# Kernel optimization log

Measured on AMD Instinct MI355X. Metric: run time of the kernel, lower is better.

## Reference

```python
import jax, jax.numpy as jnp
import numpy as np

TEMPERATURE = 0.2
EPS = 1e-8
N, D = 8192, 256
EDGE_PROB = 0.002  # ~16 neighbors per node


def setup_inputs() -> dict:
    key = jax.random.key(0)
    k1, k2, k3 = jax.random.split(key, 3)
    z_view = jax.random.normal(k1, (N, D), dtype=jnp.float32)
    z_fused = jax.random.normal(k2, (N, D), dtype=jnp.float32)
    # sparse binary fused-graph adjacency, densified (matches Gf_sparse.to_dense())
    Gf_dense = (jax.random.uniform(k3, (N, N)) < EDGE_PROB).astype(jnp.float32)
    return {"z_view": z_view, "z_fused": z_fused, "Gf_dense": Gf_dense}


def _l2_normalize(x, eps=1e-12):
    # matches F.normalize(p=2, dim=1): x / max(||x||, eps)
    norm = jnp.sqrt(jnp.sum(x * x, axis=1, keepdims=True))
    return x / jnp.maximum(norm, eps)


def reference(z_view, z_fused, Gf_dense):
    n = z_view.shape[0]
    zv = _l2_normalize(z_view)
    zf = _l2_normalize(z_fused)
    sim = jnp.matmul(zv, zf.T) / TEMPERATURE  # [N, N]
    eye = jnp.eye(n, dtype=sim.dtype)
    pos_mask = ((eye + Gf_dense) > 0).astype(sim.dtype)  # diag always 1
    neg_mask = 1.0 - pos_mask
    pos_scores = jnp.sum(sim * pos_mask, axis=1, keepdims=True) / (
        jnp.sum(pos_mask, axis=1, keepdims=True) + EPS
    )  # [N, 1]
    neg_scores = sim * neg_mask  # [N, N] (positive slots zeroed, kept as logits)
    logits = jnp.concatenate([pos_scores, neg_scores], axis=1)  # [N, N+1]
    # CrossEntropyLoss(reduction='sum') with labels == 0, then / N
    lse = jax.nn.logsumexp(logits, axis=1)
    loss = jnp.sum(lse - logits[:, 0]) / n
    return loss
```

## Files before the change

### kernel.cpp

```cpp
#include <hip/hip_runtime.h>

#define NROW 8192
#define DIM  256
#define INV_T 5.0f
#define BM 128
#define BN 128
#define CSPLIT 8
#define COLS_PER_BLOCK (NROW / CSPLIT)
#define NT 8

typedef _Float16 f16x8 __attribute__((ext_vector_type(8)));
typedef _Float16 f16x4 __attribute__((ext_vector_type(4)));
typedef float    f32x4 __attribute__((ext_vector_type(4)));
typedef unsigned long long u64;

__device__ __forceinline__ void gload_lds16(const void* g, void* l) {
  __builtin_amdgcn_global_load_lds(
      (__attribute__((address_space(1))) void*)(g),
      (__attribute__((address_space(3))) void*)(l),
      16, 0, 0);
}

__global__ __launch_bounds__(256) void norm_kernel(
    const float* __restrict__ zv, const float* __restrict__ zf,
    _Float16* __restrict__ ov, _Float16* __restrict__ of) {
  const float* in  = blockIdx.y ? zf : zv;
  _Float16*    out = blockIdx.y ? of : ov;
  int row  = blockIdx.x * 4 + (threadIdx.x >> 6);
  int lane = threadIdx.x & 63;
  float4 v = ((const float4*)(in + (size_t)row * DIM))[lane];
  float ss = v.x * v.x + v.y * v.y + v.z * v.z + v.w * v.w;
#pragma unroll
  for (int off = 1; off < 64; off <<= 1) ss += __shfl_xor(ss, off);
  float inv = 1.0f / fmaxf(sqrtf(ss), 1e-12f);
  f16x4 o;
  o.x = (_Float16)(v.x * inv);
  o.y = (_Float16)(v.y * inv);
  o.z = (_Float16)(v.z * inv);
  o.w = (_Float16)(v.w * inv);
  ((f16x4*)(out + (size_t)row * DIM))[lane] = o;
}

__global__ __launch_bounds__(256, 2) void fused_kernel(
    const _Float16* __restrict__ zv, const _Float16* __restrict__ zf,
    const float* __restrict__ Gf,
    float* __restrict__ Sp, float* __restrict__ Pp, float* __restrict__ Cp) {

  __shared__ __align__(16) _Float16 Asf[BM * DIM];
  __shared__ __align__(16) _Float16 Bs[2][BN * 32];

  const int t_   = threadIdx.x;
  const int lane = t_ & 63;
  const int w    = t_ >> 6;
  const int wr   = w >> 1;
  const int wc   = w & 1;
  const int l15  = lane & 15;
  const int kq   = lane >> 4;
  const int row0 = blockIdx.x * BM;
  const int col0 = blockIdx.y * COLS_PER_BLOCK;

#pragma unroll
  for (int c = 0; c < 16; ++c) {
    int i = c * 256 + t_;
    int row = i >> 5, cbP = i & 31;
    int cbL = cbP ^ (row & 7);
    gload_lds16(zv + (size_t)(row0 + row) * DIM + cbL * 8,
                &Asf[(size_t)(c * 256 + w * 64) * 8]);
  }

  auto stageB = [&](int buf, int s) {
    int tt = s >> 3, kk = s & 7;
    int ct0 = col0 + tt * BN;
    int k0 = kk * 32;
#pragma unroll
    for (int c = 0; c < 2; ++c) {
      int i = c * 256 + t_;
      int row = i >> 2, cbP = i & 3;
      int cbL = cbP ^ ((row >> 1) & 3);
      gload_lds16(zf + (size_t)(ct0 + row) * DIM + k0 + cbL * 8,
                  &Bs[buf][(size_t)(c * 256 + w * 64) * 8]);
    }
  };

  auto issueGf = [&](float4* q, int tt, int c0) {
    const float* base = Gf + (size_t)(row0 + wr * 64 + (lane >> 4)) * NROW
                           + col0 + tt * BN + wc * 64 + l15 * 4;
#pragma unroll
    for (int j = 0; j < 4; ++j)
      q[j] = *(const float4*)(base + (size_t)((c0 + j) * 4) * NROW);
  };

  auto maskFrom4 = [&](const float4* q) -> u64 {
    u64 e = 0;
#pragma unroll
    for (int j = 0; j < 4; ++j) {
      u64 b0 = __ballot(q[j].x > 0.0f);
      u64 b1 = __ballot(q[j].y > 0.0f);
      u64 b2 = __ballot(q[j].z > 0.0f);
      u64 b3 = __ballot(q[j].w > 0.0f);
      u64 s01 = (l15 & 1) ? b1 : b0;
      u64 s23 = (l15 & 1) ? b3 : b2;
      u64 bsel = (l15 & 2) ? s23 : s01;
      u64 ej = bsel >> (l15 >> 2);
      e = (kq == j) ? ej : e;
    }
    return e;
  };

  stageB(0, 0);

  u64 wm[4];
  {
    float4 gp[8];
#pragma unroll
    for (int c = 0; c < 8; ++c) issueGf(gp + c, 0, c);
    wm[0] = maskFrom4(gp);
    wm[1] = maskFrom4(gp + 4);
#pragma unroll
    for (int c = 0; c < 8; ++c) issueGf(gp + c, 0, 8 + c);
    wm[2] = maskFrom4(gp);
    wm[3] = maskFrom4(gp + 4);
  }
  asm volatile("s_waitcnt vmcnt(0)" ::: "memory");
  __builtin_amdgcn_s_barrier();

  f32x4 acc[4][4];
  float Sa[16], Pa[16], Ca[16];
  u64 wn[4];
  float4 gvA[4], gvB[4];
#pragma unroll
  for (int i = 0; i < 16; ++i) { Sa[i] = 0.0f; Pa[i] = 0.0f; Ca[i] = 0.0f; }

#define STEP(KK)                                                               \
  do {                                                                         \
    if ((KK) == 0) {                                                           \
      _Pragma("unroll") for (int m = 0; m < 4; ++m)                            \
          _Pragma("unroll") for (int n = 0; n < 4; ++n)                        \
              acc[m][n] = (f32x4)(0.0f);                                       \
    }                                                                          \
    f16x8 af[4], bf[4];                                                        \
    _Pragma("unroll") for (int m = 0; m < 4; ++m) {                            \
      int row = wr * 64 + m * 16 + l15;                                        \
      int cbL = ((KK) * 32 >> 3) + kq;                                         \
      int cbP = cbL ^ (row & 7);                                               \
      af[m] = *(const f16x8*)&Asf[(size_t)row * 256 + cbP * 8];                \
    }                                                                          \
    _Pragma("unroll") for (int n = 0; n < 4; ++n) {                            \
      int row = wc * 64 + n * 16 + l15;                                        \
      int cbP = kq ^ ((row >> 1) & 3);                                         \
      bf[n] = *(const f16x8*)&Bs[(KK) & 1][(size_t)row * 32 + cbP * 8];        \
    }                                                                          \
    if (t < NT - 1 || (KK) < 7) stageB(((KK) + 1) & 1, t * 8 + (KK) + 1);      \
    asm volatile("" ::: "memory");                                             \
    if ((KK) < 4) {                                                            \
      if (t < NT - 1) issueGf(((KK) & 1) ? gvB : gvA, t + 1, (KK) * 4);        \
    }                                                                          \
    asm volatile("" ::: "memory");                                             \
    _Pragma("unroll") for (int m = 0; m < 4; ++m)                              \
        _Pragma("unroll") for (int n = 0; n < 4; ++n)                          \
            acc[m][n] = __builtin_amdgcn_mfma_f32_16x16x32_f16(                \
                af[m], bf[n], acc[m][n], 0, 0, 0);                             \
    if ((KK) >= 1 && (KK) <= 4) {                                              \
      if (t < NT - 1) wn[(KK) - 1] = maskFrom4(((KK) & 1) ? gvA : gvB);        \
    }                                                                          \
    if ((KK) == 7) {                                                           \
      int ct0 = col0 + t * BN;                                                 \
      _Pragma("unroll") for (int m = 0; m < 4; ++m) {                          \
        int gi = row0 + wr * 64 + m * 16 + kq * 4;                             \
        _Pragma("unroll") for (int n = 0; n < 4; ++n) {                        \
          int gj = ct0 + wc * 64 + n * 16 + l15;                               \
          _Pragma("unroll") for (int r = 0; r < 4; ++r) {                      \
            float sim = acc[m][n][r] * INV_T;                                  \
            bool pos = (((unsigned)(wm[m] >> (r * 16 + n * 4)) & 1u) != 0u) || \
                       ((gi + r) == gj);                                       \
            float e = __expf(sim);                                             \
            int idx = m * 4 + r;                                               \
            Sa[idx] += pos ? 1.0f : e;                                         \
            Pa[idx] += pos ? sim : 0.0f;                                       \
            Ca[idx] += pos ? 1.0f : 0.0f;                                      \
          }                                                                    \
        }                                                                      \
      }                                                                        \
      if (t < NT - 1) {                                                        \
        _Pragma("unroll") for (int i = 0; i < 4; ++i) wm[i] = wn[i];           \
      }                                                                        \
    }                                                                          \
    if ((KK) < 4) {                                                            \
      if (t < NT - 1)                                                          \
        asm volatile("s_waitcnt vmcnt(4)" ::: "memory");                       \
      else                                                                     \
        asm volatile("s_waitcnt vmcnt(0)" ::: "memory");                       \
    } else {                                                                   \
      asm volatile("s_waitcnt vmcnt(0)" ::: "memory");                         \
    }                                                                          \
    __builtin_amdgcn_s_barrier();                                              \
  } while (0)

#pragma unroll 1
  for (int t = 0; t < NT; ++t) {
    STEP(0); STEP(1); STEP(2); STEP(3);
    STEP(4); STEP(5); STEP(6); STEP(7);
  }
#undef STEP

#pragma unroll
  for (int off = 1; off <= 8; off <<= 1) {
#pragma unroll
    for (int i = 0; i < 16; ++i) {
      Sa[i] += __shfl_xor(Sa[i], off);
      Pa[i] += __shfl_xor(Pa[i], off);
      Ca[i] += __shfl_xor(Ca[i], off);
    }
  }
  const int slot = blockIdx.y * 2 + wc;
#pragma unroll
  for (int i = 0; i < 16; ++i) {
    if (l15 == i) {
      int m = i >> 2, r = i & 3;
      int row = row0 + wr * 64 + m * 16 + kq * 4 + r;
      Sp[(size_t)slot * NROW + row] = Sa[i];
      Pp[(size_t)slot * NROW + row] = Pa[i];
      Cp[(size_t)slot * NROW + row] = Ca[i];
    }
  }
}

__global__ __launch_bounds__(256) void loss_partial_kernel(
    const float* __restrict__ Sp, const float* __restrict__ Pp,
    const float* __restrict__ Cp, float* __restrict__ bsum) {
  int row = blockIdx.x * 256 + threadIdx.x;
  float S = 0.0f, P = 0.0f, C = 0.0f;
#pragma unroll
  for (int s2 = 0; s2 < 16; ++s2) {
    S += Sp[(size_t)s2 * NROW + row];
    P += Pp[(size_t)s2 * NROW + row];
    C += Cp[(size_t)s2 * NROW + row];
  }
  float pos = P / (C + 1e-8f);
  float contrib = __logf(S + __expf(pos)) - pos;
#pragma unroll
  for (int off = 1; off < 64; off <<= 1) contrib += __shfl_xor(contrib, off);
  __shared__ float wsum[4];
  if ((threadIdx.x & 63) == 0) wsum[threadIdx.x >> 6] = contrib;
  __syncthreads();
  if (threadIdx.x == 0) bsum[blockIdx.x] = wsum[0] + wsum[1] + wsum[2] + wsum[3];
}

__global__ void loss_final_kernel(const float* __restrict__ bsum, float* __restrict__ out) {
  int lane = threadIdx.x;
  float v = (lane < 32) ? bsum[lane] : 0.0f;
#pragma unroll
  for (int off = 1; off < 64; off <<= 1) v += __shfl_xor(v, off);
  if (lane == 0) out[0] = v / (float)NROW;
}

extern "C" void kernel_launch(void* const* d_in, const int* in_sizes, int n_in,
                              void* d_out, int out_size, void* d_ws, size_t ws_size,
                              hipStream_t stream) {
  const float* zv = (const float*)d_in[0];
  const float* zf = (const float*)d_in[1];
  const float* Gf = (const float*)d_in[2];
  float* out = (float*)d_out;

  char* ws = (char*)d_ws;
  _Float16* zv16 = (_Float16*)ws;
  _Float16* zf16 = zv16 + (size_t)NROW * DIM;
  float* Sp = (float*)(ws + 2 * (size_t)NROW * DIM * sizeof(_Float16));
  float* Pp = Sp + 16 * (size_t)NROW;
  float* Cp = Pp + 16 * (size_t)NROW;
  float* bsum = Cp + 16 * (size_t)NROW;

  norm_kernel<<<dim3(NROW / 4, 2), 256, 0, stream>>>(zv, zf, zv16, zf16);
  fused_kernel<<<dim3(NROW / BM, CSPLIT), 256, 0, stream>>>(zv16, zf16, Gf, Sp, Pp, Cp);
  loss_partial_kernel<<<NROW / 256, 256, 0, stream>>>(Sp, Pp, Cp, bsum);
  loss_final_kernel<<<1, 64, 0, stream>>>(bsum, out);
}
```

Before: 102.6 us.

## Load B operand directly from global into registers, drop LDS staging and barriers

Removes the double-buffered LDS staging of zf tiles and the per-step barriers and waitcnts. Each wave now reads its B fragments straight from global memory (relying on L2/L1 reuse), and the Gf prefetch is restructured into fewer, larger issue points. The diagonal check moves into the mask-building ballot, and the grid is flattened to 1D so the 8 column splits of a row block are adjacent in launch order. This cuts synchronization and LDS traffic, at the risk of exposing global-load latency on the MFMA critical path with no explicit wait scheduling.

```diff
diff --git a/kernel.cpp b/kernel.cpp
--- a/kernel.cpp
+++ b/kernel.cpp
@@ -47,7 +47,6 @@
     float* __restrict__ Sp, float* __restrict__ Pp, float* __restrict__ Cp) {
 
   __shared__ __align__(16) _Float16 Asf[BM * DIM];
-  __shared__ __align__(16) _Float16 Bs[2][BN * 32];
 
   const int t_   = threadIdx.x;
   const int lane = t_ & 63;
@@ -56,8 +55,10 @@
   const int wc   = w & 1;
   const int l15  = lane & 15;
   const int kq   = lane >> 4;
-  const int row0 = blockIdx.x * BM;
-  const int col0 = blockIdx.y * COLS_PER_BLOCK;
+  const int bx   = blockIdx.x >> 3;
+  const int by   = blockIdx.x & 7;
+  const int row0 = bx * BM;
+  const int col0 = by * COLS_PER_BLOCK;
 
 #pragma unroll
   for (int c = 0; c < 16; ++c) {
@@ -68,36 +69,26 @@
                 &Asf[(size_t)(c * 256 + w * 64) * 8]);
   }
 
-  auto stageB = [&](int buf, int s) {
-    int tt = s >> 3, kk = s & 7;
-    int ct0 = col0 + tt * BN;
-    int k0 = kk * 32;
-#pragma unroll
-    for (int c = 0; c < 2; ++c) {
-      int i = c * 256 + t_;
-      int row = i >> 2, cbP = i & 3;
-      int cbL = cbP ^ ((row >> 1) & 3);
-      gload_lds16(zf + (size_t)(ct0 + row) * DIM + k0 + cbL * 8,
-                  &Bs[buf][(size_t)(c * 256 + w * 64) * 8]);
-    }
+  const float* gfbase = Gf + (size_t)(row0 + wr * 64 + kq) * NROW
+                           + col0 + wc * 64 + l15 * 4;
+
+  auto issueGf = [&](float4* q, int tt, int c0) {
+    const float* p = gfbase + (size_t)tt * BN;
+#pragma unroll
+    for (int j = 0; j < 4; ++j)
+      q[j] = *(const float4*)(p + (size_t)((c0 + j) * 4) * NROW);
   };
 
-  auto issueGf = [&](float4* q, int tt, int c0) {
-    const float* base = Gf + (size_t)(row0 + wr * 64 + (lane >> 4)) * NROW
-                           + col0 + tt * BN + wc * 64 + l15 * 4;
-#pragma unroll
-    for (int j = 0; j < 4; ++j)
-      q[j] = *(const float4*)(base + (size_t)((c0 + j) * 4) * NROW);
-  };
-
-  auto maskFrom4 = [&](const float4* q) -> u64 {
+  auto maskFrom4 = [&](const float4* q, int tt, int c0) -> u64 {
+    int bd = (row0 + wr * 64 + kq) - (col0 + tt * BN + wc * 64 + l15 * 4);
     u64 e = 0;
 #pragma unroll
     for (int j = 0; j < 4; ++j) {
-      u64 b0 = __ballot(q[j].x > 0.0f);
-      u64 b1 = __ballot(q[j].y > 0.0f);
-      u64 b2 = __ballot(q[j].z > 0.0f);
-      u64 b3 = __ballot(q[j].w > 0.0f);
+      int d = bd + (c0 + j) * 4;
+      u64 b0 = __ballot(q[j].x > 0.0f || d == 0);
+      u64 b1 = __ballot(q[j].y > 0.0f || d == 1);
+      u64 b2 = __ballot(q[j].z > 0.0f || d == 2);
+      u64 b3 = __ballot(q[j].w > 0.0f || d == 3);
       u64 s01 = (l15 & 1) ? b1 : b0;
       u64 s23 = (l15 & 1) ? b3 : b2;
       u64 bsel = (l15 & 2) ? s23 : s01;
@@ -107,22 +98,17 @@
     return e;
   };
 
-  stageB(0, 0);
-
   u64 wm[4];
   {
     float4 gp[8];
-#pragma unroll
-    for (int c = 0; c < 8; ++c) issueGf(gp + c, 0, c);
-    wm[0] = maskFrom4(gp);
-    wm[1] = maskFrom4(gp + 4);
-#pragma unroll
-    for (int c = 0; c < 8; ++c) issueGf(gp + c, 0, 8 + c);
-    wm[2] = maskFrom4(gp);
-    wm[3] = maskFrom4(gp + 4);
-  }
-  asm volatile("s_waitcnt vmcnt(0)" ::: "memory");
-  __builtin_amdgcn_s_barrier();
+    issueGf(gp, 0, 0);  issueGf(gp + 4, 0, 4);
+    wm[0] = maskFrom4(gp, 0, 0);
+    wm[1] = maskFrom4(gp + 4, 0, 4);
+    issueGf(gp, 0, 8);  issueGf(gp + 4, 0, 12);
+    wm[2] = maskFrom4(gp, 0, 8);
+    wm[3] = maskFrom4(gp + 4, 0, 12);
+  }
+  __syncthreads();
 
   f32x4 acc[4][4];
   float Sa[16], Pa[16], Ca[16];
@@ -137,42 +123,39 @@
       _Pragma("unroll") for (int m = 0; m < 4; ++m)                            \
           _Pragma("unroll") for (int n = 0; n < 4; ++n)                        \
               acc[m][n] = (f32x4)(0.0f);                                       \
-    }                                                                          \
+      if (t < NT - 1) issueGf(gvA, t + 1, 0);                                  \
+    }                                                                          \
+    if ((KK) == 1 && t < NT - 1) issueGf(gvB, t + 1, 4);                       \
     f16x8 af[4], bf[4];                                                        \
+    bf[0] = *(const f16x8*)(bp0 + (KK) * 32 + kq * 8);                         \
+    bf[1] = *(const f16x8*)(bp1 + (KK) * 32 + kq * 8);                         \
+    bf[2] = *(const f16x8*)(bp2 + (KK) * 32 + kq * 8);                         \
+    bf[3] = *(const f16x8*)(bp3 + (KK) * 32 + kq * 8);                         \
     _Pragma("unroll") for (int m = 0; m < 4; ++m) {                            \
       int row = wr * 64 + m * 16 + l15;                                        \
-      int cbL = ((KK) * 32 >> 3) + kq;                                         \
-      int cbP = cbL ^ (row & 7);                                               \
+      int cbP = ((KK) * 4 + kq) ^ (row & 7);                                   \
       af[m] = *(const f16x8*)&Asf[(size_t)row * 256 + cbP * 8];                \
     }                                                                          \
-    _Pragma("unroll") for (int n = 0; n < 4; ++n) {                            \
-      int row = wc * 64 + n * 16 + l15;                                        \
-      int cbP = kq ^ ((row >> 1) & 3);                                         \
-      bf[n] = *(const f16x8*)&Bs[(KK) & 1][(size_t)row * 32 + cbP * 8];        \
-    }                                                                          \
-    if (t < NT - 1 || (KK) < 7) stageB(((KK) + 1) & 1, t * 8 + (KK) + 1);      \
-    asm volatile("" ::: "memory");                                             \
-    if ((KK) < 4) {                                                            \
-      if (t < NT - 1) issueGf(((KK) & 1) ? gvB : gvA, t + 1, (KK) * 4);        \
-    }                                                                          \
-    asm volatile("" ::: "memory");                                             \
     _Pragma("unroll") for (int m = 0; m < 4; ++m)                              \
         _Pragma("unroll") for (int n = 0; n < 4; ++n)                          \
             acc[m][n] = __builtin_amdgcn_mfma_f32_16x16x32_f16(                \
                 af[m], bf[n], acc[m][n], 0, 0, 0);                             \
-    if ((KK) >= 1 && (KK) <= 4) {                                              \
-      if (t < NT - 1) wn[(KK) - 1] = maskFrom4(((KK) & 1) ? gvA : gvB);        \
-    }                                                                          \
+    if ((KK) == 3 && t < NT - 1) {                                             \
+      wn[0] = maskFrom4(gvA, t + 1, 0);                                        \
+      issueGf(gvA, t + 1, 8);                                                  \
+    }                                                                          \
+    if ((KK) == 4 && t < NT - 1) {                                             \
+      wn[1] = maskFrom4(gvB, t + 1, 4);                                        \
+      issueGf(gvB, t + 1, 12);                                                 \
+    }                                                                          \
+    if ((KK) == 6 && t < NT - 1) wn[2] = maskFrom4(gvA, t + 1, 8);             \
     if ((KK) == 7) {                                                           \
-      int ct0 = col0 + t * BN;                                                 \
+      if (t < NT - 1) wn[3] = maskFrom4(gvB, t + 1, 12);                       \
       _Pragma("unroll") for (int m = 0; m < 4; ++m) {                          \
-        int gi = row0 + wr * 64 + m * 16 + kq * 4;                             \
         _Pragma("unroll") for (int n = 0; n < 4; ++n) {                        \
-          int gj = ct0 + wc * 64 + n * 16 + l15;                               \
           _Pragma("unroll") for (int r = 0; r < 4; ++r) {                      \
             float sim = acc[m][n][r] * INV_T;                                  \
-            bool pos = (((unsigned)(wm[m] >> (r * 16 + n * 4)) & 1u) != 0u) || \
-                       ((gi + r) == gj);                                       \
+            bool pos = (((unsigned)(wm[m] >> (r * 16 + n * 4)) & 1u) != 0u);   \
             float e = __expf(sim);                                             \
             int idx = m * 4 + r;                                               \
             Sa[idx] += pos ? 1.0f : e;                                         \
@@ -185,19 +168,15 @@
         _Pragma("unroll") for (int i = 0; i < 4; ++i) wm[i] = wn[i];           \
       }                                                                        \
     }                                                                          \
-    if ((KK) < 4) {                                                            \
-      if (t < NT - 1)                                                          \
-        asm volatile("s_waitcnt vmcnt(4)" ::: "memory");                       \
-      else                                                                     \
-        asm volatile("s_waitcnt vmcnt(0)" ::: "memory");                       \
-    } else {                                                                   \
-      asm volatile("s_waitcnt vmcnt(0)" ::: "memory");                         \
-    }                                                                          \
-    __builtin_amdgcn_s_barrier();                                              \
   } while (0)
 
 #pragma unroll 1
   for (int t = 0; t < NT; ++t) {
+    const _Float16* brow = zf + (size_t)(col0 + t * BN + wc * 64 + l15) * DIM;
+    const _Float16* bp0 = brow;
+    const _Float16* bp1 = brow + 16 * DIM;
+    const _Float16* bp2 = brow + 32 * DIM;
+    const _Float16* bp3 = brow + 48 * DIM;
     STEP(0); STEP(1); STEP(2); STEP(3);
     STEP(4); STEP(5); STEP(6); STEP(7);
   }
@@ -212,7 +191,7 @@
       Ca[i] += __shfl_xor(Ca[i], off);
     }
   }
-  const int slot = blockIdx.y * 2 + wc;
+  const int slot = by * 2 + wc;
 #pragma unroll
   for (int i = 0; i < 16; ++i) {
     if (l15 == i) {
@@ -271,7 +250,7 @@
   float* bsum = Cp + 16 * (size_t)NROW;
 
   norm_kernel<<<dim3(NROW / 4, 2), 256, 0, stream>>>(zv, zf, zv16, zf16);
-  fused_kernel<<<dim3(NROW / BM, CSPLIT), 256, 0, stream>>>(zv16, zf16, Gf, Sp, Pp, Cp);
+  fused_kernel<<<512, 256, 0, stream>>>(zv16, zf16, Gf, Sp, Pp, Cp);
   loss_partial_kernel<<<NROW / 256, 256, 0, stream>>>(Sp, Pp, Cp, bsum);
   loss_final_kernel<<<1, 64, 0, stream>>>(bsum, out);
 }
```

After: 197.6 us. 1.93x slower.

## Batch Gf mask loads per tile, hoist B-fragment addresses, and linearize grid ordering

Applied to the files above, without the earlier changes.

Restructures the software pipeline so that all 16 Gf float4 loads for the next column tile are issued together in step 1, followed by a vmcnt(16) wait. The previous schedule spread four loads over each of steps 0-3. The B-tile stage for the next k-step now issues at the start of each step, and the swizzled B LDS addresses are precomputed once outside the loop. The grid becomes 1D with the column-split index in the low bits, so the eight blocks sharing a row block launch adjacently and can reuse the A tile in L2. The batched loads raise register pressure (16 float4 held live) at two-blocks-per-CU occupancy, and they also change the vmcnt accounting.

```diff
diff --git a/kernel.cpp b/kernel.cpp
--- a/kernel.cpp
+++ b/kernel.cpp
@@ -56,8 +56,10 @@
   const int wc   = w & 1;
   const int l15  = lane & 15;
   const int kq   = lane >> 4;
-  const int row0 = blockIdx.x * BM;
-  const int col0 = blockIdx.y * COLS_PER_BLOCK;
+  const int rb   = blockIdx.x >> 3;
+  const int cb   = blockIdx.x & 7;
+  const int row0 = rb * BM;
+  const int col0 = cb * COLS_PER_BLOCK;
 
 #pragma unroll
   for (int c = 0; c < 16; ++c) {
@@ -82,9 +84,11 @@
     }
   };
 
+  const float* gfrow = Gf + (size_t)(row0 + wr * 64 + (lane >> 4)) * NROW
+                          + col0 + wc * 64 + l15 * 4;
+
   auto issueGf = [&](float4* q, int tt, int c0) {
-    const float* base = Gf + (size_t)(row0 + wr * 64 + (lane >> 4)) * NROW
-                           + col0 + tt * BN + wc * 64 + l15 * 4;
+    const float* base = gfrow + (size_t)tt * BN;
 #pragma unroll
     for (int j = 0; j < 4; ++j)
       q[j] = *(const float4*)(base + (size_t)((c0 + j) * 4) * NROW);
@@ -124,45 +128,57 @@
   asm volatile("s_waitcnt vmcnt(0)" ::: "memory");
   __builtin_amdgcn_s_barrier();
 
+  const int brow0 = wc * 64 + 0 * 16 + l15;
+  const int brow1 = wc * 64 + 1 * 16 + l15;
+  const int brow2 = wc * 64 + 2 * 16 + l15;
+  const int brow3 = wc * 64 + 3 * 16 + l15;
+  const size_t ba0 = (size_t)brow0 * 32 + (size_t)(kq ^ ((brow0 >> 1) & 3)) * 8;
+  const size_t ba1 = (size_t)brow1 * 32 + (size_t)(kq ^ ((brow1 >> 1) & 3)) * 8;
+  const size_t ba2 = (size_t)brow2 * 32 + (size_t)(kq ^ ((brow2 >> 1) & 3)) * 8;
+  const size_t ba3 = (size_t)brow3 * 32 + (size_t)(kq ^ ((brow3 >> 1) & 3)) * 8;
+
   f32x4 acc[4][4];
   float Sa[16], Pa[16], Ca[16];
   u64 wn[4];
-  float4 gvA[4], gvB[4];
+  float4 gv[16];
 #pragma unroll
   for (int i = 0; i < 16; ++i) { Sa[i] = 0.0f; Pa[i] = 0.0f; Ca[i] = 0.0f; }
 
 #define STEP(KK)                                                               \
   do {                                                                         \
+    { int s2 = t * 8 + (KK) + 1;                                               \
+      if (s2 <= 63) stageB(s2 & 1, s2); }                                      \
     if ((KK) == 0) {                                                           \
       _Pragma("unroll") for (int m = 0; m < 4; ++m)                            \
           _Pragma("unroll") for (int n = 0; n < 4; ++n)                        \
               acc[m][n] = (f32x4)(0.0f);                                       \
     }                                                                          \
     f16x8 af[4], bf[4];                                                        \
+    bf[0] = *(const f16x8*)&Bs[(KK) & 1][ba0];                                 \
+    bf[1] = *(const f16x8*)&Bs[(KK) & 1][ba1];                                 \
+    bf[2] = *(const f16x8*)&Bs[(KK) & 1][ba2];                                 \
+    bf[3] = *(const f16x8*)&Bs[(KK) & 1][ba3];                                 \
     _Pragma("unroll") for (int m = 0; m < 4; ++m) {                            \
       int row = wr * 64 + m * 16 + l15;                                        \
-      int cbL = ((KK) * 32 >> 3) + kq;                                         \
-      int cbP = cbL ^ (row & 7);                                               \
+      int cbP = ((KK) * 4 + kq) ^ (row & 7);                                   \
       af[m] = *(const f16x8*)&Asf[(size_t)row * 256 + cbP * 8];                \
     }                                                                          \
-    _Pragma("unroll") for (int n = 0; n < 4; ++n) {                            \
-      int row = wc * 64 + n * 16 + l15;                                        \
-      int cbP = kq ^ ((row >> 1) & 3);                                         \
-      bf[n] = *(const f16x8*)&Bs[(KK) & 1][(size_t)row * 32 + cbP * 8];        \
-    }                                                                          \
-    if (t < NT - 1 || (KK) < 7) stageB(((KK) + 1) & 1, t * 8 + (KK) + 1);      \
-    asm volatile("" ::: "memory");                                             \
-    if ((KK) < 4) {                                                            \
-      if (t < NT - 1) issueGf(((KK) & 1) ? gvB : gvA, t + 1, (KK) * 4);        \
-    }                                                                          \
-    asm volatile("" ::: "memory");                                             \
+    if ((KK) == 1 && t < NT - 1) {                                             \
+      asm volatile("" ::: "memory");                                           \
+      issueGf(gv + 0,  t + 1, 0);                                              \
+      issueGf(gv + 4,  t + 1, 4);                                              \
+      issueGf(gv + 8,  t + 1, 8);                                              \
+      issueGf(gv + 12, t + 1, 12);                                             \
+      asm volatile("" ::: "memory");                                           \
+    }                                                                          \
     _Pragma("unroll") for (int m = 0; m < 4; ++m)                              \
         _Pragma("unroll") for (int n = 0; n < 4; ++n)                          \
             acc[m][n] = __builtin_amdgcn_mfma_f32_16x16x32_f16(                \
                 af[m], bf[n], acc[m][n], 0, 0, 0);                             \
-    if ((KK) >= 1 && (KK) <= 4) {                                              \
-      if (t < NT - 1) wn[(KK) - 1] = maskFrom4(((KK) & 1) ? gvA : gvB);        \
-    }                                                                          \
+    if ((KK) == 2 && t < NT - 1) wn[0] = maskFrom4(gv);                        \
+    if ((KK) == 3 && t < NT - 1) wn[1] = maskFrom4(gv + 4);                    \
+    if ((KK) == 4 && t < NT - 1) wn[2] = maskFrom4(gv + 8);                    \
+    if ((KK) == 5 && t < NT - 1) wn[3] = maskFrom4(gv + 12);                   \
     if ((KK) == 7) {                                                           \
       int ct0 = col0 + t * BN;                                                 \
       _Pragma("unroll") for (int m = 0; m < 4; ++m) {                          \
@@ -185,14 +201,10 @@
         _Pragma("unroll") for (int i = 0; i < 4; ++i) wm[i] = wn[i];           \
       }                                                                        \
     }                                                                          \
-    if ((KK) < 4) {                                                            \
-      if (t < NT - 1)                                                          \
-        asm volatile("s_waitcnt vmcnt(4)" ::: "memory");                       \
-      else                                                                     \
-        asm volatile("s_waitcnt vmcnt(0)" ::: "memory");                       \
-    } else {                                                                   \
+    if ((KK) == 1 && t < NT - 1)                                               \
+      asm volatile("s_waitcnt vmcnt(16)" ::: "memory");                        \
+    else                                                                       \
       asm volatile("s_waitcnt vmcnt(0)" ::: "memory");                         \
-    }                                                                          \
     __builtin_amdgcn_s_barrier();                                              \
   } while (0)
 
@@ -212,7 +224,7 @@
       Ca[i] += __shfl_xor(Ca[i], off);
     }
   }
-  const int slot = blockIdx.y * 2 + wc;
+  const int slot = cb * 2 + wc;
 #pragma unroll
   for (int i = 0; i < 16; ++i) {
     if (l15 == i) {
@@ -271,7 +283,7 @@
   float* bsum = Cp + 16 * (size_t)NROW;
 
   norm_kernel<<<dim3(NROW / 4, 2), 256, 0, stream>>>(zv, zf, zv16, zf16);
-  fused_kernel<<<dim3(NROW / BM, CSPLIT), 256, 0, stream>>>(zv16, zf16, Gf, Sp, Pp, Cp);
+  fused_kernel<<<512, 256, 0, stream>>>(zv16, zf16, Gf, Sp, Pp, Cp);
   loss_partial_kernel<<<NROW / 256, 256, 0, stream>>>(Sp, Pp, Cp, bsum);
   loss_final_kernel<<<1, 64, 0, stream>>>(bsum, out);
 }
```

New measurement: 123.3 us. 20.1% more time.
